# Performance work log

Measured on AMD Instinct MI355X. Metric: run time of the kernel, lower is better.

The kernel has to match this reference:

```python
import jax, jax.numpy as jnp
import numpy as np

NUM_STEPS = 5  # matches init num_steps
N_NODES = 500_000
N_EDGES = 32_000_000


def setup_inputs() -> dict:
    key = jax.random.key(0)
    k1, k2, k3 = jax.random.split(key, 3)
    prior_probs = jax.random.uniform(k1, (N_NODES,), dtype=jnp.float32)
    edge_index = jax.random.randint(k2, (2, N_EDGES), 0, N_NODES, dtype=jnp.int32)
    edge_probs = jax.random.uniform(k3, (N_EDGES,), dtype=jnp.float32)
    return {"prior_probs": prior_probs, "edge_index": edge_index, "edge_probs": edge_probs}


def reference(prior_probs, edge_index, edge_probs):
    num_nodes = prior_probs.shape[0]
    source = edge_index[0]
    target = edge_index[1]
    p_t_u = prior_probs
    prod_terms = jnp.ones_like(prior_probs)
    for _ in range(NUM_STEPS):
        # gather node activation at source, weight by edge prob, scatter-add into target
        message = edge_probs * p_t_u[source]            # [E]
        agg = jax.ops.segment_sum(message, target, num_segments=num_nodes)  # [N]
        delta = 1.0 - jnp.exp(-agg)
        new_p_t_u = prod_terms * delta
        prod_terms = prod_terms * (1.0 - new_p_t_u)
        p_t_u = new_p_t_u
    p_final = 1.0 - prod_terms + prior_probs
    return p_final.reshape(-1, 1)
```

## Files before the change

### kernel.cpp

```cpp
#include <hip/hip_runtime.h>
#include <hip/hip_fp16.h>

#define NUM_STEPS 5
typedef unsigned int u32;
typedef unsigned long long ull;
typedef int   i4nt __attribute__((ext_vector_type(4)));
typedef float f4nt __attribute__((ext_vector_type(4)));

#define RSH 10
#define RSZ 1024
#define SB  1024
#define HT  512
#define ST  512
#define NBMAX 512
#define BINS 8
#define SPLIT 2
#define SRC_BITS 19
#define SRC_MASK 0x7FFFFu

static inline size_t align256(size_t x){ return (x + 255) & ~(size_t)255; }


__global__ void init_fast(const float* __restrict__ prior, __half* __restrict__ p,
                          float* __restrict__ prod, int n){
    int i = blockIdx.x*blockDim.x + threadIdx.x;
    if(i<n){ p[i]=__float2half_rn(prior[i]); prod[i]=1.0f; }
}

__global__ void hist_kernel(const int* __restrict__ dst, long long E, int B,
                            u32* __restrict__ blk_cnt){
    extern __shared__ u32 hist[];
    int sb = blockIdx.x;
    long long E4 = E >> 2;
    long long chunk = (E4 + SB - 1)/SB;
    long long i0 = (long long)sb*chunk;
    long long i1 = i0 + chunk; if(i1 > E4) i1 = E4;
    for(int b=threadIdx.x; b<B; b+=blockDim.x) hist[b]=0;
    __syncthreads();
    const i4nt* d4 = (const i4nt*)dst;
    for(long long i=i0+threadIdx.x; i<i1; i+=blockDim.x){
        i4nt d = __builtin_nontemporal_load(d4 + i);
        atomicAdd(&hist[((u32)d.x)>>RSH], 1u);
        atomicAdd(&hist[((u32)d.y)>>RSH], 1u);
        atomicAdd(&hist[((u32)d.z)>>RSH], 1u);
        atomicAdd(&hist[((u32)d.w)>>RSH], 1u);
    }
    if(sb==0){
        for(long long e=(E4<<2)+threadIdx.x; e<E; e+=blockDim.x)
            atomicAdd(&hist[((u32)dst[e])>>RSH], 1u);
    }
    __syncthreads();
    for(int b=threadIdx.x; b<B; b+=blockDim.x) blk_cnt[(size_t)sb*B + b] = hist[b];
}

__global__ __launch_bounds__(SB) void
colscan_kernel(u32* __restrict__ blk_cnt, int B, u32* __restrict__ tot){
    __shared__ u32 s[SB];
    int b = blockIdx.x, t = threadIdx.x;
    u32 v = blk_cnt[(size_t)t*B + b];
    s[t] = v; __syncthreads();
    for(int off=1; off<SB; off<<=1){
        u32 x = (t>=off) ? s[t-off] : 0;
        __syncthreads();
        s[t] += x;
        __syncthreads();
    }
    blk_cnt[(size_t)t*B + b] = s[t] - v;
    if(t==SB-1) tot[b] = s[SB-1];
}

__global__ void basescan_kernel(const u32* __restrict__ tot, u32* __restrict__ base, int B){
    __shared__ u32 s[256];
    int t = threadIdx.x;
    u32 v0 = (2*t   < B) ? tot[2*t]   : 0;
    u32 v1 = (2*t+1 < B) ? tot[2*t+1] : 0;
    u32 sum = v0 + v1;
    s[t] = sum; __syncthreads();
    for(int off=1; off<256; off<<=1){
        u32 x = (t>=off) ? s[t-off] : 0;
        __syncthreads();
        s[t] += x;
        __syncthreads();
    }
    u32 run = s[t] - sum;
    if(2*t   < B) base[2*t]   = run;
    if(2*t+1 < B) base[2*t+1] = run + v0;
    if(t==255) base[B] = s[255];
}

__global__ __launch_bounds__(ST) void
scatter_kernel(const int* __restrict__ src, const int* __restrict__ dst,
               const float* __restrict__ ep, long long E, int B,
               const u32* __restrict__ blk_rel, const u32* __restrict__ base,
               uint2* __restrict__ edges){
    __shared__ uint2 bin[NBMAX][BINS];
    __shared__ u32 cnt[NBMAX];
    __shared__ u32 gcur[NBMAX];
    const int sb = blockIdx.x, t = threadIdx.x;
    long long E4 = E >> 2;
    long long chunk = (E4 + SB - 1)/SB;
    long long i0 = (long long)sb*chunk;
    long long i1 = i0 + chunk; if(i1 > E4) i1 = E4;
    for(int b=t; b<B; b+=ST){ cnt[b]=0; gcur[b]=base[b]+blk_rel[(size_t)sb*B+b]; }
    __syncthreads();
    const i4nt* s4=(const i4nt*)src;
    const i4nt* d4=(const i4nt*)dst;
    const f4nt* w4=(const f4nt*)ep;
    for(long long it=i0; it<i1; it+=ST){
        long long i = it + t;
        bool valid = (i < i1);
        u32 bk[4]; u32 sl[4]; uint2 pl[4];
        if(valid){
            i4nt s = __builtin_nontemporal_load(s4 + i);
            i4nt d = __builtin_nontemporal_load(d4 + i);
            f4nt w = __builtin_nontemporal_load(w4 + i);
            u32 dd;
            dd=(u32)d.x; bk[0]=dd>>RSH; pl[0]=make_uint2(((u32)s.x)|((dd&(RSZ-1))<<SRC_BITS), __float_as_uint(w.x));
            dd=(u32)d.y; bk[1]=dd>>RSH; pl[1]=make_uint2(((u32)s.y)|((dd&(RSZ-1))<<SRC_BITS), __float_as_uint(w.y));
            dd=(u32)d.z; bk[2]=dd>>RSH; pl[2]=make_uint2(((u32)s.z)|((dd&(RSZ-1))<<SRC_BITS), __float_as_uint(w.z));
            dd=(u32)d.w; bk[3]=dd>>RSH; pl[3]=make_uint2(((u32)s.w)|((dd&(RSZ-1))<<SRC_BITS), __float_as_uint(w.w));
            #pragma unroll
            for(int k=0;k<4;k++) sl[k]=atomicAdd(&cnt[bk[k]],1u);
        }
        __syncthreads();
        if(valid){
            #pragma unroll
            for(int k=0;k<4;k++){
                if(sl[k] < BINS) bin[bk[k]][sl[k]] = pl[k];
                else             edges[gcur[bk[k]] + sl[k]] = pl[k];
            }
        }
        __syncthreads();
        for(int b=t; b<B; b+=ST){
            u32 c = cnt[b];
            if(c >= BINS){
                u32 g = gcur[b];
                #pragma unroll
                for(int k2=0;k2<BINS;k2++) edges[g+k2] = bin[b][k2];
                gcur[b] = g + c;
                cnt[b]  = 0;
            }
        }
        __syncthreads();
    }
    if(sb==0){
        long long tb = E4<<2;
        int nt = (int)(E - tb);
        if(nt > 0){
            bool v = (t < nt);
            u32 bk0=0, sl0=0; uint2 pl0=make_uint2(0,0);
            if(v){
                u32 dd=(u32)dst[tb+t]; bk0=dd>>RSH;
                pl0=make_uint2(((u32)src[tb+t])|((dd&(RSZ-1))<<SRC_BITS), __float_as_uint(ep[tb+t]));
                sl0=atomicAdd(&cnt[bk0],1u);
            }
            __syncthreads();
            if(v){ if(sl0<BINS) bin[bk0][sl0]=pl0; else edges[gcur[bk0]+sl0]=pl0; }
            __syncthreads();
        }
    }
    for(int b=t; b<B; b+=ST){
        u32 c = cnt[b]; if(c > BINS) c = BINS;
        u32 g = gcur[b];
        for(u32 k2=0;k2<c;k2++) edges[g+k2] = bin[b][k2];
    }
}

__global__ __launch_bounds__(512) void
step_kernel(const uint2* __restrict__ edges, const u32* __restrict__ base,
            const __half* __restrict__ p, float* __restrict__ pacc){
    __shared__ float acc[2][RSZ];
    int blk = blockIdx.x;
    int b   = blk >> 1;
    int part= blk & 1;
    int t   = threadIdx.x;
    for(int k=t; k<RSZ; k+=512){ acc[0][k]=0.0f; acc[1][k]=0.0f; }
    __syncthreads();
    u32 e0 = base[b], e1 = base[b+1];
    u32 cnt = e1 - e0;
    u32 s0 = e0 + (cnt*(u32)part)/SPLIT;
    u32 s1 = e0 + (cnt*(u32)(part+1))/SPLIT;
    int rep = t & 1;
    u32 n = s1 - s0;
    u32 m = n >> 11;
    u32 eb = s0 + t;
    const ull* ed = (const ull*)edges;
    for(u32 it=0; it<m; ++it){
        ull r0 = __builtin_nontemporal_load(ed + eb);
        ull r1 = __builtin_nontemporal_load(ed + eb + 512);
        ull r2 = __builtin_nontemporal_load(ed + eb + 1024);
        ull r3 = __builtin_nontemporal_load(ed + eb + 1536);
        u32 x0=(u32)r0, x1=(u32)r1, x2=(u32)r2, x3=(u32)r3;
        float p0 = __half2float(p[x0 & SRC_MASK]);
        float p1 = __half2float(p[x1 & SRC_MASK]);
        float p2 = __half2float(p[x2 & SRC_MASK]);
        float p3 = __half2float(p[x3 & SRC_MASK]);
        atomicAdd(&acc[rep][x0 >> SRC_BITS], __uint_as_float((u32)(r0>>32))*p0);
        atomicAdd(&acc[rep][x1 >> SRC_BITS], __uint_as_float((u32)(r1>>32))*p1);
        atomicAdd(&acc[rep][x2 >> SRC_BITS], __uint_as_float((u32)(r2>>32))*p2);
        atomicAdd(&acc[rep][x3 >> SRC_BITS], __uint_as_float((u32)(r3>>32))*p3);
        eb += 2048;
    }
    for(u32 e=eb; e<s1; e+=512){
        ull r = __builtin_nontemporal_load(ed + e);
        u32 x = (u32)r;
        atomicAdd(&acc[rep][x >> SRC_BITS],
                  __uint_as_float((u32)(r>>32))*__half2float(p[x & SRC_MASK]));
    }
    __syncthreads();
    float* dstp = pacc + (size_t)blk * RSZ;
    for(int k=t; k<RSZ; k+=512)
        __builtin_nontemporal_store(acc[0][k] + acc[1][k], dstp + k);
}

__global__ void combine_kernel(const float* __restrict__ pacc, __half* __restrict__ p,
                               float* __restrict__ prod, const float* __restrict__ prior,
                               float* __restrict__ out, int n, int final_step){
    int i = blockIdx.x*blockDim.x + threadIdx.x;
    if(i < n){
        int b = i >> RSH, k = i & (RSZ-1);
        float a = __builtin_nontemporal_load(&pacc[(size_t)(b*SPLIT    )*RSZ + k])
                + __builtin_nontemporal_load(&pacc[(size_t)(b*SPLIT + 1)*RSZ + k]);
        float pr_old = prod[i];
        float np = pr_old * (1.0f - expf(-a));
        float pr = pr_old * (1.0f - np);
        prod[i] = pr;
        p[i] = __float2half_rn(np);
        if(final_step) out[i] = 1.0f - pr + prior[i];
    }
}


__global__ void init_kernel(const float* __restrict__ prior, float* __restrict__ p,
                            float* __restrict__ prod, float* __restrict__ agg, int n){
    int i = blockIdx.x*blockDim.x + threadIdx.x;
    if(i<n){ p[i]=prior[i]; prod[i]=1.0f; agg[i]=0.0f; }
}

__global__ void edge_kernel(const int* __restrict__ src, const int* __restrict__ dst,
                            const float* __restrict__ ep, const float* __restrict__ p,
                            float* __restrict__ agg, int e4, int e_rem, long long e4base){
    int i = blockIdx.x*blockDim.x + threadIdx.x;
    if(i < e4){
        int4   s = ((const int4*)src)[i];
        int4   t = ((const int4*)dst)[i];
        float4 w = ((const float4*)ep)[i];
        atomicAdd(&agg[t.x], w.x * p[s.x]);
        atomicAdd(&agg[t.y], w.y * p[s.y]);
        atomicAdd(&agg[t.z], w.z * p[s.z]);
        atomicAdd(&agg[t.w], w.w * p[s.w]);
    }
    if(blockIdx.x==0 && threadIdx.x < e_rem){
        long long e = e4base + threadIdx.x;
        atomicAdd(&agg[dst[e]], ep[e]*p[src[e]]);
    }
}

__global__ void node_kernel(float* __restrict__ p, float* __restrict__ prod,
                            float* __restrict__ agg, const float* __restrict__ prior,
                            float* __restrict__ out, int n, int final_step){
    int i = blockIdx.x*blockDim.x + threadIdx.x;
    if(i<n){
        float a = agg[i]; agg[i]=0.0f;
        float pr_old = prod[i];
        float np = pr_old*(1.0f - expf(-a));
        float pr = pr_old*(1.0f - np);
        prod[i]=pr; p[i]=np;
        if(final_step) out[i] = 1.0f - pr + prior[i];
    }
}


extern "C" void kernel_launch(void* const* d_in, const int* in_sizes, int n_in,
                              void* d_out, int out_size, void* d_ws, size_t ws_size,
                              hipStream_t stream){
    const float* prior = (const float*)d_in[0];
    const int*   eidx  = (const int*)d_in[1];
    const float* ep    = (const float*)d_in[2];

    const int n = in_sizes[0];
    const long long E = (long long)in_sizes[2];
    const int* src = eidx;
    const int* dst = eidx + E;
    float* out = (float*)d_out;

    const int B = (n + RSZ - 1) >> RSH;

    size_t szNh  = align256((size_t)n * 2);
    size_t szN   = align256((size_t)n * 4);
    size_t szB1  = align256((size_t)(B + 1) * 4);
    size_t szB   = align256((size_t)B * 4);
    size_t szCnt = align256((size_t)SB * B * 4);
    size_t szAcc = align256((size_t)SPLIT * B * RSZ * 4);
    size_t szE2  = align256((size_t)E * 8);

    size_t off_p    = 0;
    size_t off_prod = off_p + szNh;
    size_t off_base = off_prod + szN;
    size_t off_tot  = off_base + szB1;
    size_t off_cnt  = off_tot + szB;
    size_t off_acc  = off_cnt + szCnt;
    size_t off_edge = off_acc + szAcc;
    size_t need     = off_edge + szE2;

    char* ws = (char*)d_ws;

    if(ws_size >= need && n < (1 << SRC_BITS) && B <= NBMAX){
        __half* p    = (__half*)(ws + off_p);
        float*  prod = (float*) (ws + off_prod);
        u32*    base = (u32*)   (ws + off_base);
        u32*    tot  = (u32*)   (ws + off_tot);
        u32*    cnt  = (u32*)   (ws + off_cnt);
        float*  pacc = (float*) (ws + off_acc);
        uint2*  edges= (uint2*) (ws + off_edge);

        const int nb_n = (n + 255)/256;
        init_fast<<<nb_n, 256, 0, stream>>>(prior, p, prod, n);
        hist_kernel<<<SB, HT, (size_t)B*4, stream>>>(dst, E, B, cnt);
        colscan_kernel<<<B, SB, 0, stream>>>(cnt, B, tot);
        basescan_kernel<<<1, 256, 0, stream>>>(tot, base, B);
        scatter_kernel<<<SB, ST, 0, stream>>>(src, dst, ep, E, B, cnt, base, edges);

        for(int step=0; step<NUM_STEPS; ++step){
            step_kernel<<<B*SPLIT, 512, 0, stream>>>(edges, base, p, pacc);
            combine_kernel<<<nb_n, 256, 0, stream>>>(pacc, p, prod, prior, out, n,
                                                     step == NUM_STEPS-1 ? 1 : 0);
        }
    } else {
        float* p    = (float*)d_ws;
        float* prod = p + n;
        float* agg  = prod + n;
        const int nb_n = (n + 255)/256;
        init_kernel<<<nb_n, 256, 0, stream>>>(prior, p, prod, agg, n);
        const int e4 = (int)(E/4);
        const int e_rem = (int)(E%4);
        const long long e4base = (long long)e4*4;
        const int nb_e = (e4 + 255)/256;
        for(int step=0; step<NUM_STEPS; ++step){
            edge_kernel<<<nb_e, 256, 0, stream>>>(src, dst, ep, p, agg, e4, e_rem, e4base);
            node_kernel<<<nb_n, 256, 0, stream>>>(p, prod, agg, prior, out, n,
                                                  step == NUM_STEPS-1 ? 1 : 0);
        }
    }
}
```

Baseline: 1.221 ms.

## Retune preprocessing and step kernels: smaller blocks, more splits, plain loads

Halves the number of histogram/scatter superblocks, splits each destination bucket across four step blocks of 256 threads instead of two of 512, and unrolls the step loop to eight loads per thread. All nontemporal loads and stores become ordinary cached accesses, and the combine kernel now sums four partial accumulators. The aim is more concurrent blocks and better cache use for the edge stream. The cost is more partial-sum traffic in combine and longer per-block chunks in the scatter phase. The pacc buffer must also be sized for the larger SPLIT, which the host code may not account for.

```diff
diff --git a/kernel.cpp b/kernel.cpp
--- a/kernel.cpp
+++ b/kernel.cpp
@@ -4,17 +4,15 @@
 #define NUM_STEPS 5
 typedef unsigned int u32;
 typedef unsigned long long ull;
-typedef int   i4nt __attribute__((ext_vector_type(4)));
-typedef float f4nt __attribute__((ext_vector_type(4)));
 
 #define RSH 10
 #define RSZ 1024
-#define SB  1024
+#define SB  512
 #define HT  512
 #define ST  512
 #define NBMAX 512
 #define BINS 8
-#define SPLIT 2
+#define SPLIT 4
 #define SRC_BITS 19
 #define SRC_MASK 0x7FFFFu
 
@@ -37,9 +35,9 @@
     long long i1 = i0 + chunk; if(i1 > E4) i1 = E4;
     for(int b=threadIdx.x; b<B; b+=blockDim.x) hist[b]=0;
     __syncthreads();
-    const i4nt* d4 = (const i4nt*)dst;
+    const int4* d4 = (const int4*)dst;
     for(long long i=i0+threadIdx.x; i<i1; i+=blockDim.x){
-        i4nt d = __builtin_nontemporal_load(d4 + i);
+        int4 d = d4[i];
         atomicAdd(&hist[((u32)d.x)>>RSH], 1u);
         atomicAdd(&hist[((u32)d.y)>>RSH], 1u);
         atomicAdd(&hist[((u32)d.z)>>RSH], 1u);
@@ -103,17 +101,15 @@
     long long i1 = i0 + chunk; if(i1 > E4) i1 = E4;
     for(int b=t; b<B; b+=ST){ cnt[b]=0; gcur[b]=base[b]+blk_rel[(size_t)sb*B+b]; }
     __syncthreads();
-    const i4nt* s4=(const i4nt*)src;
-    const i4nt* d4=(const i4nt*)dst;
-    const f4nt* w4=(const f4nt*)ep;
+    const int4*   s4=(const int4*)src;
+    const int4*   d4=(const int4*)dst;
+    const float4* w4=(const float4*)ep;
     for(long long it=i0; it<i1; it+=ST){
         long long i = it + t;
         bool valid = (i < i1);
         u32 bk[4]; u32 sl[4]; uint2 pl[4];
         if(valid){
-            i4nt s = __builtin_nontemporal_load(s4 + i);
-            i4nt d = __builtin_nontemporal_load(d4 + i);
-            f4nt w = __builtin_nontemporal_load(w4 + i);
+            int4 s=s4[i]; int4 d=d4[i]; float4 w=w4[i];
             u32 dd;
             dd=(u32)d.x; bk[0]=dd>>RSH; pl[0]=make_uint2(((u32)s.x)|((dd&(RSZ-1))<<SRC_BITS), __float_as_uint(w.x));
             dd=(u32)d.y; bk[1]=dd>>RSH; pl[1]=make_uint2(((u32)s.y)|((dd&(RSZ-1))<<SRC_BITS), __float_as_uint(w.y));
@@ -166,15 +162,15 @@
     }
 }
 
-__global__ __launch_bounds__(512) void
+__global__ __launch_bounds__(256) void
 step_kernel(const uint2* __restrict__ edges, const u32* __restrict__ base,
             const __half* __restrict__ p, float* __restrict__ pacc){
     __shared__ float acc[2][RSZ];
     int blk = blockIdx.x;
-    int b   = blk >> 1;
-    int part= blk & 1;
+    int b   = blk >> 2;
+    int part= blk & 3;
     int t   = threadIdx.x;
-    for(int k=t; k<RSZ; k+=512){ acc[0][k]=0.0f; acc[1][k]=0.0f; }
+    for(int k=t; k<RSZ; k+=256){ acc[0][k]=0.0f; acc[1][k]=0.0f; }
     __syncthreads();
     u32 e0 = base[b], e1 = base[b+1];
     u32 cnt = e1 - e0;
@@ -186,31 +182,43 @@
     u32 eb = s0 + t;
     const ull* ed = (const ull*)edges;
     for(u32 it=0; it<m; ++it){
-        ull r0 = __builtin_nontemporal_load(ed + eb);
-        ull r1 = __builtin_nontemporal_load(ed + eb + 512);
-        ull r2 = __builtin_nontemporal_load(ed + eb + 1024);
-        ull r3 = __builtin_nontemporal_load(ed + eb + 1536);
+        ull r0 = ed[eb       ];
+        ull r1 = ed[eb +  256];
+        ull r2 = ed[eb +  512];
+        ull r3 = ed[eb +  768];
+        ull r4 = ed[eb + 1024];
+        ull r5 = ed[eb + 1280];
+        ull r6 = ed[eb + 1536];
+        ull r7 = ed[eb + 1792];
         u32 x0=(u32)r0, x1=(u32)r1, x2=(u32)r2, x3=(u32)r3;
+        u32 x4=(u32)r4, x5=(u32)r5, x6=(u32)r6, x7=(u32)r7;
         float p0 = __half2float(p[x0 & SRC_MASK]);
         float p1 = __half2float(p[x1 & SRC_MASK]);
         float p2 = __half2float(p[x2 & SRC_MASK]);
         float p3 = __half2float(p[x3 & SRC_MASK]);
+        float p4 = __half2float(p[x4 & SRC_MASK]);
+        float p5 = __half2float(p[x5 & SRC_MASK]);
+        float p6 = __half2float(p[x6 & SRC_MASK]);
+        float p7 = __half2float(p[x7 & SRC_MASK]);
         atomicAdd(&acc[rep][x0 >> SRC_BITS], __uint_as_float((u32)(r0>>32))*p0);
         atomicAdd(&acc[rep][x1 >> SRC_BITS], __uint_as_float((u32)(r1>>32))*p1);
         atomicAdd(&acc[rep][x2 >> SRC_BITS], __uint_as_float((u32)(r2>>32))*p2);
         atomicAdd(&acc[rep][x3 >> SRC_BITS], __uint_as_float((u32)(r3>>32))*p3);
+        atomicAdd(&acc[rep][x4 >> SRC_BITS], __uint_as_float((u32)(r4>>32))*p4);
+        atomicAdd(&acc[rep][x5 >> SRC_BITS], __uint_as_float((u32)(r5>>32))*p5);
+        atomicAdd(&acc[rep][x6 >> SRC_BITS], __uint_as_float((u32)(r6>>32))*p6);
+        atomicAdd(&acc[rep][x7 >> SRC_BITS], __uint_as_float((u32)(r7>>32))*p7);
         eb += 2048;
     }
-    for(u32 e=eb; e<s1; e+=512){
-        ull r = __builtin_nontemporal_load(ed + e);
+    for(u32 e=eb; e<s1; e+=256){
+        ull r = ed[e];
         u32 x = (u32)r;
         atomicAdd(&acc[rep][x >> SRC_BITS],
                   __uint_as_float((u32)(r>>32))*__half2float(p[x & SRC_MASK]));
     }
     __syncthreads();
     float* dstp = pacc + (size_t)blk * RSZ;
-    for(int k=t; k<RSZ; k+=512)
-        __builtin_nontemporal_store(acc[0][k] + acc[1][k], dstp + k);
+    for(int k=t; k<RSZ; k+=256) dstp[k] = acc[0][k] + acc[1][k];
 }
 
 __global__ void combine_kernel(const float* __restrict__ pacc, __half* __restrict__ p,
@@ -219,8 +227,10 @@
     int i = blockIdx.x*blockDim.x + threadIdx.x;
     if(i < n){
         int b = i >> RSH, k = i & (RSZ-1);
-        float a = __builtin_nontemporal_load(&pacc[(size_t)(b*SPLIT    )*RSZ + k])
-                + __builtin_nontemporal_load(&pacc[(size_t)(b*SPLIT + 1)*RSZ + k]);
+        float a = 0.0f;
+        #pragma unroll
+        for(int q=0;q<SPLIT;q++)
+            a += pacc[(size_t)(b*SPLIT + q)*RSZ + k];
         float pr_old = prod[i];
         float np = pr_old * (1.0f - expf(-a));
         float pr = pr_old * (1.0f - np);
@@ -322,7 +332,7 @@
         scatter_kernel<<<SB, ST, 0, stream>>>(src, dst, ep, E, B, cnt, base, edges);
 
         for(int step=0; step<NUM_STEPS; ++step){
-            step_kernel<<<B*SPLIT, 512, 0, stream>>>(edges, base, p, pacc);
+            step_kernel<<<B*SPLIT, 256, 0, stream>>>(edges, base, p, pacc);
             combine_kernel<<<nb_n, 256, 0, stream>>>(pacc, p, prod, prior, out, n,
                                                      step == NUM_STEPS-1 ? 1 : 0);
         }
```

After: 1.141 ms. -6.5%, faster.
